# Optimization experiments

Hardware: AMD Instinct MI355X
Metric: run time of the kernel (lower is better)

## Reference

```python
import jax, jax.numpy as jnp
import numpy as np
import math

V, H, L, NH, I, E, K, S, B = 32000, 1024, 4, 16, 2816, 8, 2, 2048, 1
HD = H // NH
MOE_IDX = 2
EPS = 1e-6
THETA = 10000.0
AUX_COEF, Z_COEF = 0.01, 0.001


def setup_inputs() -> dict:
    key = jax.random.key(0)
    ks = jax.random.split(key, 20)
    std = 0.02
    n_dense = L - 1  # layers 0,1,3
    inp = {
        "input_ids": jax.random.randint(ks[0], (B, S), 0, V, dtype=jnp.int64),
        "embed": jax.random.normal(ks[1], (V, H), jnp.float32) * std,
        "ln1_w": jnp.ones((L, H), jnp.float32),
        "ln2_w": jnp.ones((L, H), jnp.float32),
        "wq": jax.random.normal(ks[2], (L, H, H), jnp.float32) * std,
        "wk": jax.random.normal(ks[3], (L, H, H), jnp.float32) * std,
        "wv": jax.random.normal(ks[4], (L, H, H), jnp.float32) * std,
        "wo": jax.random.normal(ks[5], (L, H, H), jnp.float32) * std,
        "dense_gate": jax.random.normal(ks[6], (n_dense, H, I), jnp.float32) * std,
        "dense_up": jax.random.normal(ks[7], (n_dense, H, I), jnp.float32) * std,
        "dense_down": jax.random.normal(ks[8], (n_dense, I, H), jnp.float32) * std,
        "router_w": jax.random.normal(ks[9], (H, E), jnp.float32) * std,
        "moe_gate": jax.random.normal(ks[10], (E, H, I), jnp.float32) * std,
        "moe_up": jax.random.normal(ks[11], (E, H, I), jnp.float32) * std,
        "moe_down": jax.random.normal(ks[12], (E, I, H), jnp.float32) * std,
        "final_norm_w": jnp.ones((H,), jnp.float32),
    }
    return inp


def rmsnorm(x, w):
    return x * jax.lax.rsqrt(jnp.mean(x * x, -1, keepdims=True) + EPS) * w


def rope_tables():
    inv_freq = 1.0 / (THETA ** (jnp.arange(0, HD, 2, dtype=jnp.float32) / HD))
    ang = jnp.arange(S, dtype=jnp.float32)[:, None] * inv_freq[None, :]  # [S, HD/2]
    return jnp.cos(ang), jnp.sin(ang)


def apply_rope(x, cos, sin):
    # x: [B,S,NH,HD]; cos/sin [S,HD/2] -> broadcast [1,S,1,HD/2]
    c = cos[None, :, None, :]
    s = sin[None, :, None, :]
    x1, x2 = jnp.split(x, 2, axis=-1)
    return jnp.concatenate([x1 * c - x2 * s, x2 * c + x1 * s], axis=-1)


def attention(x, wq, wk, wv, wo, cos, sin, mask):
    q = (x @ wq).reshape(B, S, NH, HD)
    k = (x @ wk).reshape(B, S, NH, HD)
    v = (x @ wv).reshape(B, S, NH, HD)
    q = apply_rope(q, cos, sin)
    k = apply_rope(k, cos, sin)
    scores = jnp.einsum("bqhd,bkhd->bhqk", q, k) / math.sqrt(HD)
    scores = jnp.where(mask, scores, jnp.finfo(scores.dtype).min)
    p = jax.nn.softmax(scores, axis=-1)
    o = jnp.einsum("bhqk,bkhd->bqhd", p, v).reshape(B, S, H)
    return o @ wo


def swiglu_mlp(x, wg, wu, wd):
    return (jax.nn.silu(x @ wg) * (x @ wu)) @ wd


def moe_layer(x, router_w, wg, wu, wd):
    T = B * S
    xf = x.reshape(T, H)
    rl = xf @ router_w  # [T,E]
    probs = jax.nn.softmax(rl, axis=-1)
    vals, idx = jax.lax.top_k(probs, K)  # [T,K]
    vals = vals / jnp.sum(vals, axis=-1, keepdims=True)
    rows = jnp.arange(T)[:, None]
    w = jnp.zeros((T, E), xf.dtype).at[rows, idx].set(vals)  # dense combine weights
    g = jnp.einsum("th,ehi->tei", xf, wg)
    u = jnp.einsum("th,ehi->tei", xf, wu)
    a = jax.nn.silu(g) * u
    y = jnp.einsum("tei,eih,te->th", a, wd, w)
    # load-balancing aux loss (Switch-style) + router z-loss
    sel = jnp.zeros((T, E), xf.dtype).at[rows, idx].add(1.0)
    f = jnp.mean(sel, axis=0)
    P = jnp.mean(probs, axis=0)
    aux = AUX_COEF * E * jnp.sum(f * P)
    z = Z_COEF * jnp.mean(jax.nn.logsumexp(rl, axis=-1) ** 2)
    return y.reshape(B, S, H), aux + z


def reference(input_ids, embed, ln1_w, ln2_w, wq, wk, wv, wo,
              dense_gate, dense_up, dense_down,
              router_w, moe_gate, moe_up, moe_down, final_norm_w):
    cos, sin = rope_tables()
    mask = jnp.tril(jnp.ones((S, S), bool))[None, None, :, :]
    h = embed[input_ids]  # [B,S,H]
    total_aux = jnp.float32(0.0)
    n_moe = 0
    d = 0  # dense layer counter
    for li in range(L):
        res = h
        hn = rmsnorm(h, ln1_w[li])
        h = res + attention(hn, wq[li], wk[li], wv[li], wo[li], cos, sin, mask)
        res = h
        hn = rmsnorm(h, ln2_w[li])
        if li == MOE_IDX:
            y, aux = moe_layer(hn, router_w, moe_gate, moe_up, moe_down)
            total_aux = total_aux + aux
            n_moe += 1
        else:
            y = swiglu_mlp(hn, dense_gate[d], dense_up[d], dense_down[d])
            d += 1
        h = res + y
    h = rmsnorm(h, final_norm_w)
    logits = h @ embed.T  # tied lm_head
    aux_loss = total_aux / n_moe
    return logits, aux_loss
```

## Files before the change

### kernel.cpp

```cpp
#include <hip/hip_runtime.h>
#include <hip/hip_bf16.h>
#include <math.h>

#define SEQ 2048
#define HID 1024
#define NHEAD 16
#define HDIM 64
#define IDIM 2816
#define NEXP 8
#define VOCAB 32000

#define ASTRIDE 144

typedef float f32x4v __attribute__((ext_vector_type(4)));
typedef __bf16 bf16x8v __attribute__((ext_vector_type(8)));
typedef __bf16 bf16x4v __attribute__((ext_vector_type(4)));

__device__ __forceinline__ bf16x8v cvt8(const float4& a, const float4& b) {
  bf16x8v r;
  r[0] = (__bf16)a.x; r[1] = (__bf16)a.y; r[2] = (__bf16)a.z; r[3] = (__bf16)a.w;
  r[4] = (__bf16)b.x; r[5] = (__bf16)b.y; r[6] = (__bf16)b.z; r[7] = (__bf16)b.w;
  return r;
}

#define MFMA(a, b, c) __builtin_amdgcn_mfma_f32_16x16x32_bf16(a, b, c, 0, 0, 0)

__device__ __forceinline__ void gld_lds16(const void* g, void* l) {
  __builtin_amdgcn_global_load_lds(
      (const __attribute__((address_space(1))) unsigned int*)(unsigned long long)g,
      (__attribute__((address_space(3))) unsigned int*)(unsigned int)(unsigned long long)l,
      16, 0, 0);
}

__global__ __launch_bounds__(256) void wsplit_t_kernel(
    const float* __restrict__ W, __bf16* __restrict__ WH, __bf16* __restrict__ WL,
    int K, int N)
{
  __shared__ float tile[64][65];
  const int tid = threadIdx.x;
  const size_t zofs = (size_t)blockIdx.z * K * N;
  const int n0 = blockIdx.x * 64, k0 = blockIdx.y * 64;
#pragma unroll
  for (int r = 0; r < 4; ++r) {
    int kk = (tid >> 4) + r * 16;
    int nn = (tid & 15) * 4;
    float4 v = *(const float4*)(W + zofs + (size_t)(k0 + kk) * N + n0 + nn);
    tile[kk][nn] = v.x; tile[kk][nn + 1] = v.y;
    tile[kk][nn + 2] = v.z; tile[kk][nn + 3] = v.w;
  }
  __syncthreads();
  const int nn = tid >> 2;
  const int kk = (tid & 3) * 16;
  __bf16* dh = WH + zofs + (size_t)(n0 + nn) * K + k0 + kk;
  __bf16* dl = WL + zofs + (size_t)(n0 + nn) * K + k0 + kk;
  bf16x8v h0, l0, h1, l1;
#pragma unroll
  for (int j = 0; j < 8; ++j) {
    float f = tile[kk + j][nn];
    __bf16 hb = (__bf16)f; h0[j] = hb; l0[j] = (__bf16)(f - (float)hb);
    f = tile[kk + 8 + j][nn];
    hb = (__bf16)f; h1[j] = hb; l1[j] = (__bf16)(f - (float)hb);
  }
  *(bf16x8v*)dh = h0; *(bf16x8v*)(dh + 8) = h1;
  *(bf16x8v*)dl = l0; *(bf16x8v*)(dl + 8) = l1;
}

__global__ __launch_bounds__(256) void wsplit_th_kernel(
    const float* __restrict__ W, __bf16* __restrict__ WH, int K, int N)
{
  __shared__ float tile[64][65];
  const int tid = threadIdx.x;
  const size_t zofs = (size_t)blockIdx.z * K * N;
  const int n0 = blockIdx.x * 64, k0 = blockIdx.y * 64;
#pragma unroll
  for (int r = 0; r < 4; ++r) {
    int kk = (tid >> 4) + r * 16;
    int nn = (tid & 15) * 4;
    float4 v = *(const float4*)(W + zofs + (size_t)(k0 + kk) * N + n0 + nn);
    tile[kk][nn] = v.x; tile[kk][nn + 1] = v.y;
    tile[kk][nn + 2] = v.z; tile[kk][nn + 3] = v.w;
  }
  __syncthreads();
  const int nn = tid >> 2;
  const int kk = (tid & 3) * 16;
  __bf16* dh = WH + zofs + (size_t)(n0 + nn) * K + k0 + kk;
  bf16x8v h0, h1;
#pragma unroll
  for (int j = 0; j < 8; ++j) {
    h0[j] = (__bf16)tile[kk + j][nn];
    h1[j] = (__bf16)tile[kk + 8 + j][nn];
  }
  *(bf16x8v*)dh = h0; *(bf16x8v*)(dh + 8) = h1;
}

__global__ __launch_bounds__(256) void esplit_kernel(
    const float* __restrict__ E, __bf16* __restrict__ EH)
{
  size_t i = ((size_t)blockIdx.x * 256 + threadIdx.x) * 8;
  float4 a = *(const float4*)(E + i);
  float4 b = *(const float4*)(E + i + 4);
  *(bf16x8v*)(EH + i) = cvt8(a, b);
}

template<bool COMP, bool ACCUM, int BM, int BN, bool XSWZ>
__global__ __launch_bounds__(256) void gemm_bt_kernel(
    const __bf16* __restrict__ Ah, const __bf16* __restrict__ Al,
    const __bf16* __restrict__ B0h, const __bf16* __restrict__ B0l,
    const __bf16* __restrict__ B1h, const __bf16* __restrict__ B1l,
    const __bf16* __restrict__ B2h, const __bf16* __restrict__ B2l,
    float* __restrict__ C0, float* __restrict__ C1, float* __restrict__ C2,
    int M, int N, int Kd)
{
  const __bf16* __restrict__ Bh = (blockIdx.z == 0) ? B0h : (blockIdx.z == 1 ? B1h : B2h);
  const __bf16* __restrict__ Bl = (blockIdx.z == 0) ? B0l : (blockIdx.z == 1 ? B1l : B2l);
  float* __restrict__ C         = (blockIdx.z == 0) ? C0 : (blockIdx.z == 1 ? C1 : C2);
  constexpr int ATILE = BM * 64;
  constexpr int BTILE = BN * 64;
  constexpr int MFR = BM / 32;
  constexpr int NFR = BN / 32;
  constexpr int SBUF = COMP ? 2 * (ATILE + BTILE) : (ATILE + BTILE);
  __shared__ __align__(16) char smem[2 * SBUF];
  const int tid = threadIdx.x;
  int bm, bn;
  if (XSWZ) {
    int id = blockIdx.x;
    int xcd = id & 7;
    int j = id >> 3;
    if (BM == 128) {
      bm = j & 15;
      bn = xcd * 32 + (j >> 4);
    } else {
      bm = j & 31;
      bn = xcd * 32 + (j >> 5);
    }
    if (bn >= N / BN) return;
  } else {
    bm = blockIdx.y;
// ... 13 lines not shown
#pragma unroll
    for (int c = wid; c < BM / 16; c += 4) {
      size_t gofs = (size_t)(bm * BM + c * 16 + lrow) * Kd + k0 + lcol;
      gld_lds16(Ah + gofs, AsH + c * 1024);
      if (COMP) gld_lds16(Al + gofs, AsL + c * 1024);
    }
#pragma unroll
    for (int c = wid; c < BN / 16; c += 4) {
      size_t gofs = (size_t)(bn * BN + c * 16 + lrow) * Kd + k0 + lcol;
      gld_lds16(Bh + gofs, BsH + c * 1024);
      if (COMP) gld_lds16(Bl + gofs, BsL + c * 1024);
    }
  };

  f32x4v acc[MFR][NFR];
  const f32x4v z4 = {0.f, 0.f, 0.f, 0.f};
#pragma unroll
  for (int i = 0; i < MFR; ++i)
#pragma unroll
    for (int j2 = 0; j2 < NFR; ++j2) acc[i][j2] = z4;

  stage(smem, 0);
  int cur = 0;
  for (int k0 = 0; k0 < Kd; k0 += 32) {
    __syncthreads();
    char* buf = smem + cur * SBUF;
    if (k0 + 32 < Kd) stage(smem + (cur ^ 1) * SBUF, k0 + 32);
    char* AsH = buf;
    char* BsH = buf + ATILE;
    char* AsL = COMP ? buf + ATILE + BTILE : buf;
    char* BsL = COMP ? buf + 2 * ATILE + BTILE : buf + ATILE;

    bf16x8v ah[MFR], al[MFR], bh4[NFR], bl4[NFR];
#pragma unroll
    for (int i = 0; i < MFR; ++i) {
      int r = wm + (i << 4) + lr;
      int off = r * 64 + (kh << 4);
      ah[i] = *(const bf16x8v*)(AsH + off);
      if (COMP) al[i] = *(const bf16x8v*)(AsL + off);
    }
#pragma unroll
    for (int i = 0; i < NFR; ++i) {
      int r = wn + (i << 4) + lr;
      int off = r * 64 + (kh << 4);
      bh4[i] = *(const bf16x8v*)(BsH + off);
      if (COMP) bl4[i] = *(const bf16x8v*)(BsL + off);
    }
#pragma unroll
    for (int mi = 0; mi < MFR; ++mi)
#pragma unroll
      for (int ni = 0; ni < NFR; ++ni) {
        if (COMP) {
          acc[mi][ni] = MFMA(al[mi], bh4[ni], acc[mi][ni]);
          acc[mi][ni] = MFMA(ah[mi], bl4[ni], acc[mi][ni]);
        }
        acc[mi][ni] = MFMA(ah[mi], bh4[ni], acc[mi][ni]);
      }
    cur ^= 1;
  }

  const int cr0 = kh << 2;
#pragma unroll
  for (int mi = 0; mi < MFR; ++mi)
#pragma unroll
    for (int ni = 0; ni < NFR; ++ni)
#pragma unroll
      for (int r = 0; r < 4; ++r) {
        int row = bm * BM + wm + (mi << 4) + cr0 + r;
        int col = bn * BN + wn + (ni << 4) + lr;
        size_t idx = (size_t)row * N + col;
        if (ACCUM) C[idx] += acc[mi][ni][r];
        else       C[idx] = acc[mi][ni][r];
      }
}

template<bool COMP>
__global__ __launch_bounds__(256) void gemm_qkv_kernel(
    const __bf16* __restrict__ Ah, const __bf16* __restrict__ Al,
    const __bf16* __restrict__ Bqh, const __bf16* __restrict__ Bql,
    const __bf16* __restrict__ Bkh, const __bf16* __restrict__ Bkl,
    const __bf16* __restrict__ Bvh, const __bf16* __restrict__ Bvl,
    __bf16* __restrict__ QH, __bf16* __restrict__ QL,
    __bf16* __restrict__ KH, __bf16* __restrict__ KL,
    float* __restrict__ Vout,
    const float* __restrict__ CT, const float* __restrict__ ST)
{
  const __bf16* __restrict__ Bh = (blockIdx.z == 0) ? Bqh : (blockIdx.z == 1 ? Bkh : Bvh);
  const __bf16* __restrict__ Bl = (blockIdx.z == 0) ? Bql : (blockIdx.z == 1 ? Bkl : Bvl);
  constexpr int ATILE = 64 * 64;
  constexpr int BTILE = 128 * 64;
  constexpr int SBUF = COMP ? 2 * (ATILE + BTILE) : (ATILE + BTILE);
  __shared__ __align__(16) char smem[2 * SBUF];
  const int tid = threadIdx.x;
  const int bm = blockIdx.y, bn = blockIdx.x;
  const int wid = tid >> 6, lane = tid & 63;
  const int wm = (wid >> 1) << 5, wn = (wid & 1) << 6;
  const int lr = lane & 15, kh = lane >> 4;
  const int lrow = lane >> 2;
  const int lcol = (lane & 3) << 3;

  auto stage = [&](char* buf, int k0) {
    char* AsH = buf;
    char* BsH = buf + ATILE;
    char* AsL = COMP ? buf + ATILE + BTILE : buf;
    char* BsL = COMP ? buf + 2 * ATILE + BTILE : buf + ATILE;
    {
      int c = wid;
      size_t gofs = (size_t)(bm * 64 + c * 16 + lrow) * HID + k0 + lcol;
      gld_lds16(Ah + gofs, AsH + c * 1024);
      if (COMP) gld_lds16(Al + gofs, AsL + c * 1024);
    }
#pragma unroll
    for (int c = wid; c < 8; c += 4) {
      size_t gofs = (size_t)(bn * 128 + c * 16 + lrow) * HID + k0 + lcol;
      gld_lds16(Bh + gofs, BsH + c * 1024);
      if (COMP) gld_lds16(Bl + gofs, BsL + c * 1024);
    }
  };

  f32x4v acc[2][4];
  const f32x4v z4 = {0.f, 0.f, 0.f, 0.f};
#pragma unroll
  for (int i = 0; i < 2; ++i)
#pragma unroll
    for (int j2 = 0; j2 < 4; ++j2) acc[i][j2] = z4;

  stage(smem, 0);
  int cur = 0;
  for (int k0 = 0; k0 < HID; k0 += 32) {
    __syncthreads();
    char* buf = smem + cur * SBUF;
    if (k0 + 32 < HID) stage(smem + (cur ^ 1) * SBUF, k0 + 32);
    char* AsH = buf;
    char* BsH = buf + ATILE;
    char* AsL = COMP ? buf + ATILE + BTILE : buf;
    char* BsL = COMP ? buf + 2 * ATILE + BTILE : buf + ATILE;

    bf16x8v ah2[2], al2[2], bh4[4], bl4[4];
#pragma unroll
    for (int i = 0; i < 2; ++i) {
      int r = wm + (i << 4) + lr;
      int off = r * 64 + (kh << 4);
      ah2[i] = *(const bf16x8v*)(AsH + off);
      if (COMP) al2[i] = *(const bf16x8v*)(AsL + off);
    }
#pragma unroll
    for (int i = 0; i < 4; ++i) {
      int r = wn + (i << 4) + lr;
      int off = r * 64 + (kh << 4);
      bh4[i] = *(const bf16x8v*)(BsH + off);
      if (COMP) bl4[i] = *(const bf16x8v*)(BsL + off);
    }
#pragma unroll
    for (int mi = 0; mi < 2; ++mi)
#pragma unroll
      for (int ni = 0; ni < 4; ++ni) {
        if (COMP) {
          acc[mi][ni] = MFMA(al2[mi], bh4[ni], acc[mi][ni]);
          acc[mi][ni] = MFMA(ah2[mi], bl4[ni], acc[mi][ni]);
        }
        acc[mi][ni] = MFMA(ah2[mi], bh4[ni], acc[mi][ni]);
      }
    cur ^= 1;
  }

  const int cr0 = kh << 2;
  if (blockIdx.z == 2) {
#pragma unroll
    for (int mi = 0; mi < 2; ++mi)
#pragma unroll
      for (int ni = 0; ni < 4; ++ni)
#pragma unroll
        for (int r = 0; r < 4; ++r) {
          int row = bm * 64 + wm + (mi << 4) + cr0 + r;
          int col = bn * 128 + wn + (ni << 4) + lr;
          Vout[(size_t)row * HID + col] = acc[mi][ni][r];
        }
  } else {
    const float scale = (blockIdx.z == 0) ? 0.125f : 1.0f;
    __bf16* OH = (blockIdx.z == 0) ? QH : KH;
    __bf16* OL = (blockIdx.z == 0) ? QL : KL;
#pragma unroll
    for (int mi = 0; mi < 2; ++mi)
#pragma unroll
      for (int ni = 0; ni < 2; ++ni)
#pragma unroll
        for (int r = 0; r < 4; ++r) {
          int row = bm * 64 + wm + (mi << 4) + cr0 + r;
          int col = bn * 128 + wn + (ni << 4) + lr;
          int i = col & 31;
          float c = CT[row * 32 + i], sn = ST[row * 32 + i];
          float x1 = acc[mi][ni][r];
          float x2 = acc[mi][ni + 2][r];
          float o1 = (x1 * c - x2 * sn) * scale;
          float o2 = (x2 * c + x1 * sn) * scale;
          size_t ofs = (size_t)row * HID + col;
          __bf16 h1 = (__bf16)o1;
          OH[ofs] = h1; OL[ofs] = (__bf16)(o1 - (float)h1);
          __bf16 h2 = (__bf16)o2;
          OH[ofs + 32] = h2; OL[ofs + 32] = (__bf16)(o2 - (float)h2);
        }
  }
}

template<bool COMP>
__global__ __launch_bounds__(256) void gemm_dgu_kernel(
    const __bf16* __restrict__ Ah, const __bf16* __restrict__ Al,
    const __bf16* __restrict__ BGh, const __bf16* __restrict__ BGl,
    const __bf16* __restrict__ BUh, const __bf16* __restrict__ BUl,
    __bf16* __restrict__ GH, __bf16* __restrict__ GL)
{
  constexpr int SBUF = COMP ? 24576 : 12288;
  __shared__ __align__(16) char smem[2 * SBUF];
  const int tid = threadIdx.x;
  const int bn = blockIdx.x, bm = blockIdx.y;
  const int wid = tid >> 6, lane = tid & 63;
  const int wm = (wid >> 1) << 5, wn = (wid & 1) << 5;
  const int lr = lane & 15, kh = lane >> 4;
  const int lrow = lane >> 2;
  const int lcol = (lane & 3) << 3;

  auto stage = [&](char* buf, int k0) {
    char* AsH = buf;
    char* BgH = buf + 4096;
    char* BuH = buf + 8192;
    char* AsL = COMP ? buf + 12288 : buf;
    char* BgL = COMP ? buf + 16384 : buf;
    char* BuL = COMP ? buf + 20480 : buf;
    int c = wid;
    size_t aofs = (size_t)(bm * 64 + c * 16 + lrow) * HID + k0 + lcol;
    gld_lds16(Ah + aofs, AsH + c * 1024);
    if (COMP) gld_lds16(Al + aofs, AsL + c * 1024);
    size_t bofs = (size_t)(bn * 64 + c * 16 + lrow) * HID + k0 + lcol;
    gld_lds16(BGh + bofs, BgH + c * 1024);
    gld_lds16(BUh + bofs, BuH + c * 1024);
    if (COMP) {
      gld_lds16(BGl + bofs, BgL + c * 1024);
      gld_lds16(BUl + bofs, BuL + c * 1024);
    }
  };

  f32x4v accg[2][2], accu[2][2];
  const f32x4v z4 = {0.f, 0.f, 0.f, 0.f};
#pragma unroll
  for (int i = 0; i < 2; ++i)
#pragma unroll
    for (int j = 0; j < 2; ++j) { accg[i][j] = z4; accu[i][j] = z4; }

  stage(smem, 0);
  int cur = 0;
  for (int k0 = 0; k0 < HID; k0 += 32) {
    __syncthreads();
    char* buf = smem + cur * SBUF;
    if (k0 + 32 < HID) stage(smem + (cur ^ 1) * SBUF, k0 + 32);
    char* AsH = buf;
    char* BgH = buf + 4096;
    char* BuH = buf + 8192;
    char* AsL = COMP ? buf + 12288 : buf;
    char* BgL = COMP ? buf + 16384 : buf;
    char* BuL = COMP ? buf + 20480 : buf;

    bf16x8v af[2], afl[2], bg4[2], bgl4[2], bu4[2], bul4[2];
#pragma unroll
    for (int i = 0; i < 2; ++i) {
      int r = wm + (i << 4) + lr;
      int off = r * 64 + (kh << 4);
      af[i] = *(const bf16x8v*)(AsH + off);
      if (COMP) afl[i] = *(const bf16x8v*)(AsL + off);
    }
#pragma unroll
    for (int i = 0; i < 2; ++i) {
      int r = wn + (i << 4) + lr;
      int off = r * 64 + (kh << 4);
      bg4[i] = *(const bf16x8v*)(BgH + off);
      bu4[i] = *(const bf16x8v*)(BuH + off);
      if (COMP) {
        bgl4[i] = *(const bf16x8v*)(BgL + off);
        bul4[i] = *(const bf16x8v*)(BuL + off);
      }
    }
#pragma unroll
    for (int mi = 0; mi < 2; ++mi)
#pragma unroll
      for (int ni = 0; ni < 2; ++ni) {
        if (COMP) {
          accg[mi][ni] = MFMA(afl[mi], bg4[ni], accg[mi][ni]);
          accg[mi][ni] = MFMA(af[mi], bgl4[ni], accg[mi][ni]);
        }
        accg[mi][ni] = MFMA(af[mi], bg4[ni], accg[mi][ni]);
        if (COMP) {
          accu[mi][ni] = MFMA(afl[mi], bu4[ni], accu[mi][ni]);
          accu[mi][ni] = MFMA(af[mi], bul4[ni], accu[mi][ni]);
        }
        accu[mi][ni] = MFMA(af[mi], bu4[ni], accu[mi][ni]);
      }
    cur ^= 1;
  }

  const int cr0 = kh << 2;
#pragma unroll
  for (int mi = 0; mi < 2; ++mi)
#pragma unroll
    for (int ni = 0; ni < 2; ++ni)
#pragma unroll
      for (int r = 0; r < 4; ++r) {
        int row = bm * 64 + wm + (mi << 4) + cr0 + r;
        int col = bn * 64 + wn + (ni << 4) + lr;
        float gv = accg[mi][ni][r];
        float uv = accu[mi][ni][r];
        float a = gv / (1.f + __expf(-gv)) * uv;
        size_t idx = (size_t)row * IDIM + col;
        __bf16 hb = (__bf16)a;
        GH[idx] = hb;
        GL[idx] = (__bf16)(a - (float)hb);
      }
}

__global__ __launch_bounds__(256) void vtsplit_kernel(
    const float* __restrict__ V, __bf16* __restrict__ VTH, __bf16* __restrict__ VTL)
{
  __shared__ float tile[64][65];
  const int tid = threadIdx.x;
  const int s0 = blockIdx.x * 64;
  const int head = blockIdx.y;
#pragma unroll
  for (int r = 0; r < 4; ++r) {
    int ss = (tid >> 4) + r * 16;
    int dd = (tid & 15) * 4;
    float4 v = *(const float4*)(V + (size_t)(s0 + ss) * HID + head * 64 + dd);
    tile[ss][dd] = v.x; tile[ss][dd + 1] = v.y;
    tile[ss][dd + 2] = v.z; tile[ss][dd + 3] = v.w;
  }
  __syncthreads();
#pragma unroll
  for (int half = 0; half < 2; ++half) {
    const int d = (tid >> 3) + (half << 5);
    const int c = tid & 7;
    bf16x8v hv, lv;
#pragma unroll
    for (int j = 0; j < 8; ++j) {
      float f = tile[c * 8 + j][d];
      __bf16 hb = (__bf16)f;
      hv[j] = hb; lv[j] = (__bf16)(f - (float)hb);
    }
    size_t dst = (size_t)(head * 64 + d) * SEQ + s0 + c * 8;
    *(bf16x8v*)(VTH + dst) = hv;
    *(bf16x8v*)(VTL + dst) = lv;
  }
}

__global__ __launch_bounds__(256) void attn_flash_kernel(
    const __bf16* __restrict__ QH, const __bf16* __restrict__ QL,
    const __bf16* __restrict__ KH, const __bf16* __restrict__ KL,
    const __bf16* __restrict__ VTH, const __bf16* __restrict__ VTL,
    __bf16* __restrict__ OH, __bf16* __restrict__ OL)
{
  const int head = blockIdx.y;
  const int tid = threadIdx.x, wid = tid >> 6, lane = tid & 63;
  const int lr = lane & 15, kh = lane >> 4;
  __shared__ __align__(16) char KsH[64 * ASTRIDE], KsL[64 * ASTRIDE];
  __shared__ __align__(16) char VtH[64 * ASTRIDE], VtL[64 * ASTRIDE];
  __shared__ __align__(16) char PsH[4][16 * ASTRIDE], PsL[4][16 * ASTRIDE];

#pragma unroll
  for (int seg = 0; seg < 2; ++seg) {
    const int qt = seg ? (31 - (int)blockIdx.x) : (int)blockIdx.x;

    const size_t qofs = (size_t)(qt * 64 + wid * 16 + lr) * HID + head * HDIM;
    const bf16x8v qfh0 = *(const bf16x8v*)(QH + qofs + (kh << 3));
    const bf16x8v qfh1 = *(const bf16x8v*)(QH + qofs + 32 + (kh << 3));
    const bf16x8v qfl0 = *(const bf16x8v*)(QL + qofs + (kh << 3));
    const bf16x8v qfl1 = *(const bf16x8v*)(QL + qofs + 32 + (kh << 3));

    float m_run[4], l_run[4];
    f32x4v oacc[4];
    const f32x4v z4 = {0.f, 0.f, 0.f, 0.f};
#pragma unroll
    for (int i = 0; i < 4; ++i) { m_run[i] = -1e30f; l_run[i] = 0.f; oacc[i] = z4; }

    for (int kt = 0; kt <= qt; ++kt) {
      __syncthreads();
#pragma unroll
      for (int p = 0; p < 2; ++p) {
        int g = tid + (p << 8);
        int r = g >> 3;
        int c = g & 7;
        int off = r * ASTRIDE + (c << 4);
        const size_t kofs = (size_t)(kt * 64 + r) * HID + head * HDIM + (c << 3);
        *(bf16x8v*)(KsH + off) = *(const bf16x8v*)(KH + kofs);
        *(bf16x8v*)(KsL + off) = *(const bf16x8v*)(KL + kofs);
        const size_t vofs = (size_t)(head * 64 + r) * SEQ + kt * 64 + (c << 3);
        *(bf16x8v*)(VtH + off) = *(const bf16x8v*)(VTH + vofs);
        *(bf16x8v*)(VtL + off) = *(const bf16x8v*)(VTL + vofs);
      }
      __syncthreads();

      float sv[4][4];
#pragma unroll
      for (int stt = 0; stt < 4; ++stt) {
        int r = (stt << 4) + lr;
        int off0 = r * ASTRIDE + (kh << 4);
        int off1 = off0 + 64;
        bf16x8v kfh0 = *(const bf16x8v*)(KsH + off0);
        bf16x8v kfl0 = *(const bf16x8v*)(KsL + off0);
        bf16x8v kfh1 = *(const bf16x8v*)(KsH + off1);
        bf16x8v kfl1 = *(const bf16x8v*)(KsL + off1);
        f32x4v s = z4;
        s = MFMA(qfl0, kfh0, s);
        s = MFMA(qfh0, kfl0, s);
        s = MFMA(qfh0, kfh0, s);
        s = MFMA(qfl1, kfh1, s);
        s = MFMA(qfh1, kfl1, s);
        s = MFMA(qfh1, kfh1, s);
        int key = kt * 64 + (stt << 4) + lr;
#pragma unroll
        for (int rr = 0; rr < 4; ++rr) {
          int qr = qt * 64 + wid * 16 + (kh << 2) + rr;
          sv[stt][rr] = (key <= qr) ? s[rr] : -1e30f;
        }
      }

#pragma unroll
      for (int rr = 0; rr < 4; ++rr) {
        float mx = fmaxf(fmaxf(sv[0][rr], sv[1][rr]), fmaxf(sv[2][rr], sv[3][rr]));
#pragma unroll
        for (int d = 1; d < 16; d <<= 1) mx = fmaxf(mx, __shfl_xor(mx, d));
        float mnew = fmaxf(m_run[rr], mx);
        float scl = __expf(m_run[rr] - mnew);
        float pv[4];
#pragma unroll
        for (int stt = 0; stt < 4; ++stt) pv[stt] = __expf(sv[stt][rr] - mnew);
        float rs = pv[0] + pv[1] + pv[2] + pv[3];
#pragma unroll
        for (int d = 1; d < 16; d <<= 1) rs += __shfl_xor(rs, d);
        l_run[rr] = l_run[rr] * scl + rs;
        m_run[rr] = mnew;
#pragma unroll
        for (int n = 0; n < 4; ++n) oacc[n][rr] *= scl;
        int qlr = (kh << 2) + rr;
#pragma unroll
        for (int stt = 0; stt < 4; ++stt) {
          __bf16 hb = (__bf16)pv[stt];
          __bf16 lb = (__bf16)(pv[stt] - (float)hb);
          int off = qlr * ASTRIDE + (((stt << 4) + lr) << 1);
          *(__bf16*)(PsH[wid] + off) = hb;
          *(__bf16*)(PsL[wid] + off) = lb;
        }
      }

      int poff0 = lr * ASTRIDE + (kh << 4);
      int poff1 = poff0 + 64;
      bf16x8v pah0 = *(const bf16x8v*)(PsH[wid] + poff0);
      bf16x8v pal0 = *(const bf16x8v*)(PsL[wid] + poff0);
      bf16x8v pah1 = *(const bf16x8v*)(PsH[wid] + poff1);
      bf16x8v pal1 = *(const bf16x8v*)(PsL[wid] + poff1);
#pragma unroll
      for (int n = 0; n < 4; ++n) {
        int vr = (n << 4) + lr;
        int voff0 = vr * ASTRIDE + (kh << 4);
        int voff1 = voff0 + 64;
        bf16x8v vfh0 = *(const bf16x8v*)(VtH + voff0);
        bf16x8v vfl0 = *(const bf16x8v*)(VtL + voff0);
        bf16x8v vfh1 = *(const bf16x8v*)(VtH + voff1);
        bf16x8v vfl1 = *(const bf16x8v*)(VtL + voff1);
        oacc[n] = MFMA(pal0, vfh0, oacc[n]);
        oacc[n] = MFMA(pah0, vfl0, oacc[n]);
        oacc[n] = MFMA(pah0, vfh0, oacc[n]);
        oacc[n] = MFMA(pal1, vfh1, oacc[n]);
        oacc[n] = MFMA(pah1, vfl1, oacc[n]);
        oacc[n] = MFMA(pah1, vfh1, oacc[n]);
      }
    }

#pragma unroll
    for (int n = 0; n < 4; ++n)
#pragma unroll
      for (int rr = 0; rr < 4; ++rr) {
        int qr = qt * 64 + wid * 16 + (kh << 2) + rr;
        size_t ofs = (size_t)qr * HID + head * HDIM + (n << 4) + lr;
        float val = oacc[n][rr] / l_run[rr];
        __bf16 hb = (__bf16)val;
        OH[ofs] = hb;
        OL[ofs] = (__bf16)(val - (float)hb);
      }
  }
}

__global__ __launch_bounds__(256) void gemm_moe_guf_kernel(
    const __bf16* __restrict__ Xh,
    const __bf16* __restrict__ MGH, const __bf16* __restrict__ MUH,
    __bf16* __restrict__ A2, const float* __restrict__ W,
    const int* __restrict__ list, const int* __restrict__ cnt8,
    const int* __restrict__ off8)
{
  const int e = blockIdx.z;
  const int cnt = cnt8[e];
  const int bn = blockIdx.x, bm = blockIdx.y;
  if (bm * 128 >= cnt) return;
  const int base = off8[e];
  constexpr int SBUF = 16384;
  __shared__ __align__(16) char smem[2 * SBUF];
  const int tid = threadIdx.x;
  const int wid = tid >> 6, lane = tid & 63;
  const int wm = (wid >> 1) << 6, wn = (wid & 1) << 5;
  const int lr = lane & 15, kh = lane >> 4;
  const int lrow = lane >> 2;
  const int lcol = (lane & 3) << 3;

  auto stage = [&](char* buf, int k0) {
    char* AsB = buf;
    char* BgB = buf + 8192;
    char* BuB = buf + 12288;
#pragma unroll
    for (int c = wid; c < 8; c += 4) {
      int rg = bm * 128 + c * 16 + lrow;
      int tok = list[e * SEQ + (rg < cnt ? rg : cnt - 1)];
      gld_lds16(Xh + (size_t)tok * HID + k0 + lcol, AsB + c * 1024);
    }
    {
      int c = wid;
      size_t wofs = (size_t)(e * IDIM + bn * 64 + c * 16 + lrow) * HID + k0 + lcol;
      gld_lds16(MGH + wofs, BgB + c * 1024);
      gld_lds16(MUH + wofs, BuB + c * 1024);
    }
  };

  f32x4v accg[4][2], accu[4][2];
  const f32x4v z4 = {0.f, 0.f, 0.f, 0.f};
#pragma unroll
  for (int i = 0; i < 4; ++i)
#pragma unroll
    for (int j = 0; j < 2; ++j) { accg[i][j] = z4; accu[i][j] = z4; }

  stage(smem, 0);
  int cur = 0;
  for (int k0 = 0; k0 < HID; k0 += 32) {
    __syncthreads();
    char* buf = smem + cur * SBUF;
    if (k0 + 32 < HID) stage(smem + (cur ^ 1) * SBUF, k0 + 32);
    char* AsB = buf;
    char* BgB = buf + 8192;
    char* BuB = buf + 12288;

    bf16x8v af[4], bg4[2], bu4[2];
#pragma unroll
    for (int i = 0; i < 4; ++i) {
      int r = wm + (i << 4) + lr;
      af[i] = *(const bf16x8v*)(AsB + r * 64 + (kh << 4));
    }
#pragma unroll
    for (int i = 0; i < 2; ++i) {
      int r = wn + (i << 4) + lr;
      bg4[i] = *(const bf16x8v*)(BgB + r * 64 + (kh << 4));
      bu4[i] = *(const bf16x8v*)(BuB + r * 64 + (kh << 4));
// ... 71 lines not shown
    for (int j = 0; j < 2; ++j) acc[i][j] = z4;

  stage(smem, 0);
  int cur = 0;
  for (int k0 = 0; k0 < IDIM; k0 += 32) {
    __syncthreads();
    char* buf = smem + cur * SBUF;
    if (k0 + 32 < IDIM) stage(smem + (cur ^ 1) * SBUF, k0 + 32);
    char* AsB = buf;
    char* BsB = buf + 8192;

    bf16x8v af[4], bfv[2];
#pragma unroll
    for (int i = 0; i < 4; ++i) {
      int r = wm + (i << 4) + lr;
      af[i] = *(const bf16x8v*)(AsB + r * 64 + (kh << 4));
    }
#pragma unroll
    for (int i = 0; i < 2; ++i) {
      int r = wn + (i << 4) + lr;
      bfv[i] = *(const bf16x8v*)(BsB + r * 64 + (kh << 4));
    }
#pragma unroll
    for (int mi = 0; mi < 4; ++mi)
#pragma unroll
      for (int ni = 0; ni < 2; ++ni)
        acc[mi][ni] = MFMA(af[mi], bfv[ni], acc[mi][ni]);
    cur ^= 1;
  }

  const int cr0 = kh << 2;
#pragma unroll
  for (int mi = 0; mi < 4; ++mi)
#pragma unroll
    for (int ni = 0; ni < 2; ++ni)
#pragma unroll
      for (int r = 0; r < 4; ++r) {
        int row = bm * 128 + wm + (mi << 4) + cr0 + r;
        if (row < cnt) {
          int col = bn * 64 + wn + (ni << 4) + lr;
          Y2[(size_t)(base + row) * HID + col] = acc[mi][ni][r];
        }
      }
}

__global__ __launch_bounds__(256) void moe_scatter_kernel(
    const int* __restrict__ tokpair, const int* __restrict__ off8,
    const float* __restrict__ Y2, float* __restrict__ H)
{
  const int t = blockIdx.x;
  const int i = threadIdx.x;
  int p0 = tokpair[t * 2], p1 = tokpair[t * 2 + 1];
  size_t r0 = off8[p0 >> 16] + (p0 & 0xffff);
  size_t r1 = off8[p1 >> 16] + (p1 & 0xffff);
  float4 a = ((const float4*)(Y2 + r0 * HID))[i];
  float4 b = ((const float4*)(Y2 + r1 * HID))[i];
  float4 hv = ((float4*)(H + (size_t)t * HID))[i];
  hv.x = (hv.x + a.x) + b.x;
  hv.y = (hv.y + a.y) + b.y;
  hv.z = (hv.z + a.z) + b.z;
  hv.w = (hv.w + a.w) + b.w;
  ((float4*)(H + (size_t)t * HID))[i] = hv;
}

__global__ void tables_kernel(float* __restrict__ CT, float* __restrict__ ST)
{
  int idx = blockIdx.x * 256 + threadIdx.x;
  int s = idx >> 5, i = idx & 31;
  double inv = exp(-log(10000.0) * (double)i / 32.0);
  double ang = (double)s * inv;
  CT[idx] = (float)cos(ang);
  ST[idx] = (float)sin(ang);
}

__global__ __launch_bounds__(256) void embed_kernel(
    const int* __restrict__ ids, const float* __restrict__ E, float* __restrict__ H)
{
  int t = blockIdx.x;
  int id = ids[t];
  ((float4*)(H + (size_t)t * HID))[threadIdx.x] =
      ((const float4*)(E + (size_t)id * HID))[threadIdx.x];
}

__global__ __launch_bounds__(256) void rmsnorm_kernel(
    const float* __restrict__ X, const float* __restrict__ W,
    float* __restrict__ O, __bf16* __restrict__ OHb, __bf16* __restrict__ OLb)
{
  int t = blockIdx.x;
  int tid = threadIdx.x;
  float4 v = ((const float4*)(X + (size_t)t * HID))[tid];
  float ss = v.x * v.x + v.y * v.y + v.z * v.z + v.w * v.w;
#pragma unroll
  for (int d = 1; d < 64; d <<= 1) ss += __shfl_xor(ss, d);
  __shared__ float red[4];
  if ((tid & 63) == 0) red[tid >> 6] = ss;
  __syncthreads();
  float tot = red[0] + red[1] + red[2] + red[3];
  float inv = 1.0f / sqrtf(tot * (1.0f / 1024.0f) + 1e-6f);
  float4 w = ((const float4*)W)[tid];
  float4 r;
  r.x = v.x * inv * w.x; r.y = v.y * inv * w.y;
  r.z = v.z * inv * w.z; r.w = v.w * inv * w.w;
  ((float4*)(O + (size_t)t * HID))[tid] = r;
  float f[4] = {r.x, r.y, r.z, r.w};
  bf16x4v hv, lv;
#pragma unroll
  for (int j = 0; j < 4; ++j) {
    __bf16 hb = (__bf16)f[j];
    hv[j] = hb; lv[j] = (__bf16)(f[j] - (float)hb);
  }
  *(bf16x4v*)(OHb + (size_t)t * HID + tid * 4) = hv;
  *(bf16x4v*)(OLb + (size_t)t * HID + tid * 4) = lv;
}

__global__ __launch_bounds__(256) void router_kernel(
    const float* __restrict__ X, const float* __restrict__ RW, float* __restrict__ RL)
{
  int wid = threadIdx.x >> 6, lane = threadIdx.x & 63;
  int t = blockIdx.x * 4 + wid;
  const float* x = X + (size_t)t * HID;
  float a0 = 0, a1 = 0, a2 = 0, a3 = 0, a4 = 0, a5 = 0, a6 = 0, a7 = 0;
  for (int hh = lane; hh < HID; hh += 64) {
    float xv = x[hh];
    float4 f0 = *(const float4*)(RW + hh * 8);
    float4 f1 = *(const float4*)(RW + hh * 8 + 4);
    a0 += xv * f0.x; a1 += xv * f0.y; a2 += xv * f0.z; a3 += xv * f0.w;
    a4 += xv * f1.x; a5 += xv * f1.y; a6 += xv * f1.z; a7 += xv * f1.w;
  }
#pragma unroll
  for (int d = 1; d < 64; d <<= 1) {
    a0 += __shfl_xor(a0, d); a1 += __shfl_xor(a1, d);
    a2 += __shfl_xor(a2, d); a3 += __shfl_xor(a3, d);
    a4 += __shfl_xor(a4, d); a5 += __shfl_xor(a5, d);
    a6 += __shfl_xor(a6, d); a7 += __shfl_xor(a7, d);
  }
  if (lane == 0) {
    float* dst = RL + (size_t)t * 8;
    dst[0] = a0; dst[1] = a1; dst[2] = a2; dst[3] = a3;
    dst[4] = a4; dst[5] = a5; dst[6] = a6; dst[7] = a7;
  }
}

__global__ void zero_kernel(float* __restrict__ p, int n)
{
  int i = threadIdx.x;
  if (i < n) p[i] = 0.f;
}

__global__ void zeroi_kernel(int* __restrict__ p, int n)
{
  int i = threadIdx.x;
  if (i < n) p[i] = 0;
}

__global__ __launch_bounds__(256) void topk_kernel(
    const float* __restrict__ RL, float* __restrict__ W, float* __restrict__ AUX)
{
  int t = blockIdx.x * 256 + threadIdx.x;
  int lane = threadIdx.x & 63;
  float r[8];
#pragma unroll
  for (int e = 0; e < 8; ++e) r[e] = RL[t * 8 + e];
  float mx = r[0];
#pragma unroll
  for (int e = 1; e < 8; ++e) mx = fmaxf(mx, r[e]);
  float p[8];
  float se = 0.f;
#pragma unroll
  for (int e = 0; e < 8; ++e) { p[e] = __expf(r[e] - mx); se += p[e]; }
  float inv = 1.f / se;
#pragma unroll
  for (int e = 0; e < 8; ++e) p[e] *= inv;
  float lse = logf(se) + mx;
  int i1 = 0; float v1 = p[0];
#pragma unroll
  for (int e = 1; e < 8; ++e) if (p[e] > v1) { v1 = p[e]; i1 = e; }
  int i2 = -1; float v2 = -1.f;
#pragma unroll
  for (int e = 0; e < 8; ++e) if (e != i1 && p[e] > v2) { v2 = p[e]; i2 = e; }
  float s12 = v1 + v2;
#pragma unroll
  for (int e = 0; e < 8; ++e)
    W[t * 8 + e] = (e == i1) ? v1 / s12 : ((e == i2) ? v2 / s12 : 0.f);
#pragma unroll
  for (int e = 0; e < 8; ++e) {
    float fe = ((i1 == e) ? 1.f : 0.f) + ((i2 == e) ? 1.f : 0.f);
// ... 36 lines not shown
  }
}

__global__ void prefix_kernel(const int* __restrict__ cnt, int* __restrict__ off)
{
  if (threadIdx.x == 0) {
    int s = 0;
    for (int e = 0; e < 8; ++e) { off[e] = s; s += cnt[e]; }
  }
}

extern "C" void kernel_launch(void* const* d_in, const int* in_sizes, int n_in,
                              void* d_out, int out_size, void* d_ws, size_t ws_size,
                              hipStream_t stream)
{
  const int*   ids   = (const int*)d_in[0];
  const float* embed = (const float*)d_in[1];
  const float* ln1   = (const float*)d_in[2];
  const float* ln2   = (const float*)d_in[3];
  const float* wq    = (const float*)d_in[4];
  const float* wk    = (const float*)d_in[5];
  const float* wv    = (const float*)d_in[6];
  const float* wo    = (const float*)d_in[7];
  const float* dg    = (const float*)d_in[8];
  const float* du    = (const float*)d_in[9];
  const float* dd    = (const float*)d_in[10];
  const float* rw    = (const float*)d_in[11];
  const float* mg    = (const float*)d_in[12];
  const float* mu    = (const float*)d_in[13];
  const float* md    = (const float*)d_in[14];
  const float* fin   = (const float*)d_in[15];
  float* out = (float*)d_out;

  char* ws = (char*)d_ws;
  float* h    = (float*)(ws + 0);
  float* hn   = (float*)(ws + 8388608);
  float* q    = (float*)(ws + 16777216);
  float* k    = (float*)(ws + 25165824);
  float* v    = (float*)(ws + 33554432);
  __bf16* oh  = (__bf16*)(ws + 41943040);
  __bf16* ol  = (__bf16*)(ws + 46137344);
  float* g    = (float*)(ws + 50331648);
  float* u    = (float*)(ws + 73400320);
  float* ct   = (float*)(ws + 96468992);
  float* st   = (float*)(ws + 96731136);
  float* rl   = (float*)(ws + 96993280);
  float* wmoe = (float*)(ws + 97058816);
  float* aux  = (float*)(ws + 97124352);
  int*   cnt  = (int*)  (ws + 97124608);
  int*   list = (int*)  (ws + 97124864);
  int*   tokp = (int*)  (ws + 97190400);
  int*   off8 = (int*)  (ws + 97206784);
  __bf16* wqh = (__bf16*)(ws + 97320960);
  __bf16* wql = (__bf16*)(ws + 105709568);
  __bf16* wkh = (__bf16*)(ws + 114098176);
  __bf16* wkl = (__bf16*)(ws + 122486784);
  __bf16* wvh = (__bf16*)(ws + 130875392);
  __bf16* wvl = (__bf16*)(ws + 139264000);
  __bf16* woh = (__bf16*)(ws + 147652608);
  __bf16* wol = (__bf16*)(ws + 156041216);
  __bf16* dgh = (__bf16*)(ws + 164429824);
  __bf16* dgl = (__bf16*)(ws + 181731328);
  __bf16* duh = (__bf16*)(ws + 199032832);
  __bf16* dul = (__bf16*)(ws + 216334336);
  __bf16* ddh = (__bf16*)(ws + 233635840);
  __bf16* ddl = (__bf16*)(ws + 250937344);
  __bf16* eh  = (__bf16*)(ws + 268238848);
  __bf16* hnh = (__bf16*)(ws + 333774848);
  __bf16* hnl = (__bf16*)(ws + 337969152);
  __bf16* gh  = (__bf16*)(ws + 342163456);
  __bf16* gl  = (__bf16*)(ws + 353697792);
  __bf16* mgh = (__bf16*)(ws + 365232128);
  __bf16* muh = (__bf16*)(ws + 411369472);
  __bf16* mdh = (__bf16*)(ws + 457506816);
  __bf16* qh  = (__bf16*)g;
  __bf16* ql  = (__bf16*)((char*)g + 4194304);
  __bf16* kbh = (__bf16*)((char*)g + 8388608);
  __bf16* kbl = (__bf16*)((char*)g + 12582912);
  __bf16* vth = (__bf16*)u;
  __bf16* vtl = (__bf16*)((char*)u + 4194304);
  __bf16* a2  = (__bf16*)g;
  float*  y2  = u;

  wsplit_t_kernel<<<dim3(16, 16, 4), 256, 0, stream>>>(wq, wqh, wql, HID, HID);
  wsplit_t_kernel<<<dim3(16, 16, 4), 256, 0, stream>>>(wk, wkh, wkl, HID, HID);
  wsplit_t_kernel<<<dim3(16, 16, 4), 256, 0, stream>>>(wv, wvh, wvl, HID, HID);
  wsplit_t_kernel<<<dim3(16, 16, 4), 256, 0, stream>>>(wo, woh, wol, HID, HID);
  wsplit_t_kernel<<<dim3(44, 16, 3), 256, 0, stream>>>(dg, dgh, dgl, HID, IDIM);
  wsplit_t_kernel<<<dim3(44, 16, 3), 256, 0, stream>>>(du, duh, dul, HID, IDIM);
  wsplit_t_kernel<<<dim3(16, 44, 3), 256, 0, stream>>>(dd, ddh, ddl, IDIM, HID);
  wsplit_th_kernel<<<dim3(44, 16, 8), 256, 0, stream>>>(mg, mgh, HID, IDIM);
  wsplit_th_kernel<<<dim3(44, 16, 8), 256, 0, stream>>>(mu, muh, HID, IDIM);
  wsplit_th_kernel<<<dim3(16, 44, 8), 256, 0, stream>>>(md, mdh, IDIM, HID);
  esplit_kernel<<<16000, 256, 0, stream>>>(embed, eh);

  tables_kernel<<<256, 256, 0, stream>>>(ct, st);
  embed_kernel<<<SEQ, 256, 0, stream>>>(ids, embed, h);

  for (int li = 0; li < 4; ++li) {
    const bool comp = (li <= 2);
    rmsnorm_kernel<<<SEQ, 256, 0, stream>>>(h, ln1 + li * HID, hn, hnh, hnl);
    size_t wofs = (size_t)li * HID * HID;
    if (comp)
      gemm_qkv_kernel<true><<<dim3(8, 32, 3), 256, 0, stream>>>(
          hnh, hnl, wqh + wofs, wql + wofs, wkh + wofs, wkl + wofs,
          wvh + wofs, wvl + wofs, qh, ql, kbh, kbl, v, ct, st);
    else
      gemm_qkv_kernel<false><<<dim3(8, 32, 3), 256, 0, stream>>>(
          hnh, hnh, wqh + wofs, wqh + wofs, wkh + wofs, wkh + wofs,
          wvh + wofs, wvh + wofs, qh, ql, kbh, kbl, v, ct, st);

    vtsplit_kernel<<<dim3(32, 16), 256, 0, stream>>>(v, vth, vtl);

    attn_flash_kernel<<<dim3(16, 16), 256, 0, stream>>>(
        qh, ql, kbh, kbl, vth, vtl, oh, ol);

    if (comp)
      gemm_bt_kernel<true, true, 64, 64, false><<<dim3(16, 32, 1), 256, 0, stream>>>(
          oh, ol, woh + wofs, wol + wofs, woh + wofs, wol + wofs,
          woh + wofs, wol + wofs, h, h, h, SEQ, HID, HID);
    else
      gemm_bt_kernel<false, true, 64, 64, false><<<dim3(16, 32, 1), 256, 0, stream>>>(
          oh, oh, woh + wofs, woh + wofs, woh + wofs, woh + wofs,
          woh + wofs, woh + wofs, h, h, h, SEQ, HID, HID);

    rmsnorm_kernel<<<SEQ, 256, 0, stream>>>(h, ln2 + li * HID, hn, hnh, hnl);
    if (li == 2) {
      router_kernel<<<512, 256, 0, stream>>>(hn, rw, rl);
      zero_kernel<<<1, 32, 0, stream>>>(aux, 17);
      topk_kernel<<<8, 256, 0, stream>>>(rl, wmoe, aux);
      aux_kernel<<<1, 1, 0, stream>>>(aux, out);
      zeroi_kernel<<<1, 32, 0, stream>>>(cnt, 8);
      build_list_kernel<<<8, 256, 0, stream>>>(wmoe, cnt, list, tokp);
      prefix_kernel<<<1, 64, 0, stream>>>(cnt, off8);
      gemm_moe_guf_kernel<<<dim3(44, 16, 8), 256, 0, stream>>>(
          hnh, mgh, muh, a2, wmoe, list, cnt, off8);
      gemm_moe_down2_kernel<<<dim3(16, 16, 8), 256, 0, stream>>>(
          a2, mdh, y2, cnt, off8);
      moe_scatter_kernel<<<SEQ, 256, 0, stream>>>(tokp, off8, y2, h);
    } else {
      int d = (li < 2) ? li : li - 1;
      size_t go = (size_t)d * HID * IDIM;
      if (comp)
        gemm_dgu_kernel<true><<<dim3(44, 32), 256, 0, stream>>>(
            hnh, hnl, dgh + go, dgl + go, duh + go, dul + go, gh, gl);
      else
        gemm_dgu_kernel<false><<<dim3(44, 32), 256, 0, stream>>>(
            hnh, hnh, dgh + go, dgh + go, duh + go, duh + go, gh, gl);
      if (comp)
        gemm_bt_kernel<true, true, 64, 64, false><<<dim3(16, 32, 1), 256, 0, stream>>>(
            gh, gl, ddh + go, ddl + go, ddh + go, ddl + go,
            ddh + go, ddl + go, h, h, h, SEQ, HID, IDIM);
      else
        gemm_bt_kernel<false, true, 64, 64, false><<<dim3(16, 32, 1), 256, 0, stream>>>(
            gh, gh, ddh + go, ddh + go, ddh + go, ddh + go,
            ddh + go, ddh + go, h, h, h, SEQ, HID, IDIM);
    }
  }
  rmsnorm_kernel<<<SEQ, 256, 0, stream>>>(h, fin, hn, hnh, hnl);
  gemm_bt_kernel<false, false, 128, 128, true><<<dim3(4096, 1, 1), 256, 0, stream>>>(
      hnh, hnh, eh, eh, eh, eh, eh, eh, out, out, out, SEQ, VOCAB, HID);
}
```

Measured before the change: 1.711 ms.

## Fuse V transpose-split into QKV GEMM, merge weight splits, trim rmsnorm writes

The V projection epilogue now goes through LDS, transposes, and writes the bf16 hi/lo V^T buffers itself, so the separate vtsplit kernel and the fp32 V round trip are gone. The four per-matrix Q/K/V/O weight split launches become one kernel launch. rmsnorm skips its fp32 output except where the router needs it. s_setprio hints are added around the MFMA sections in the attention kernel. The shared-memory buffer grows to 32KB for the non-compensated variant, which can lower occupancy, and the hardcoded byte offsets in the weight split assume a contiguous buffer layout.

```diff
diff --git a/kernel.cpp b/kernel.cpp
--- a/kernel.cpp
+++ b/kernel.cpp
@@ -53,6 +53,45 @@
   const int kk = (tid & 3) * 16;
   __bf16* dh = WH + zofs + (size_t)(n0 + nn) * K + k0 + kk;
   __bf16* dl = WL + zofs + (size_t)(n0 + nn) * K + k0 + kk;
+  bf16x8v h0, l0, h1, l1;
+#pragma unroll
+  for (int j = 0; j < 8; ++j) {
+    float f = tile[kk + j][nn];
+    __bf16 hb = (__bf16)f; h0[j] = hb; l0[j] = (__bf16)(f - (float)hb);
+    f = tile[kk + 8 + j][nn];
+    hb = (__bf16)f; h1[j] = hb; l1[j] = (__bf16)(f - (float)hb);
+  }
+  *(bf16x8v*)dh = h0; *(bf16x8v*)(dh + 8) = h1;
+  *(bf16x8v*)dl = l0; *(bf16x8v*)(dl + 8) = l1;
+}
+
+__global__ __launch_bounds__(256) void wsplit_qkvo_kernel(
+    const float* __restrict__ W0, const float* __restrict__ W1,
+    const float* __restrict__ W2, const float* __restrict__ W3,
+    __bf16* __restrict__ WHbase)
+{
+  const int z = blockIdx.z;
+  const int li = z & 3, sel = z >> 2;
+  const float* W = (sel == 0) ? W0 : (sel == 1) ? W1 : (sel == 2) ? W2 : W3;
+  const size_t lofs = (size_t)li * HID * HID;
+  __bf16* WH = (__bf16*)((char*)WHbase + (size_t)sel * 16777216) + lofs;
+  __bf16* WL = (__bf16*)((char*)WHbase + (size_t)sel * 16777216 + 8388608) + lofs;
+  __shared__ float tile[64][65];
+  const int tid = threadIdx.x;
+  const int n0 = blockIdx.x * 64, k0 = blockIdx.y * 64;
+#pragma unroll
+  for (int r = 0; r < 4; ++r) {
+    int kk = (tid >> 4) + r * 16;
+    int nn = (tid & 15) * 4;
+    float4 v = *(const float4*)(W + lofs + (size_t)(k0 + kk) * HID + n0 + nn);
+    tile[kk][nn] = v.x; tile[kk][nn + 1] = v.y;
+    tile[kk][nn + 2] = v.z; tile[kk][nn + 3] = v.w;
+  }
+  __syncthreads();
+  const int nn = tid >> 2;
+  const int kk = (tid & 3) * 16;
+  __bf16* dh = WH + (size_t)(n0 + nn) * HID + k0 + kk;
+  __bf16* dl = WL + (size_t)(n0 + nn) * HID + k0 + kk;
   bf16x8v h0, l0, h1, l1;
 #pragma unroll
   for (int j = 0; j < 8; ++j) {
@@ -232,7 +271,7 @@
     const __bf16* __restrict__ Bvh, const __bf16* __restrict__ Bvl,
     __bf16* __restrict__ QH, __bf16* __restrict__ QL,
     __bf16* __restrict__ KH, __bf16* __restrict__ KL,
-    float* __restrict__ Vout,
+    __bf16* __restrict__ VTH, __bf16* __restrict__ VTL,
     const float* __restrict__ CT, const float* __restrict__ ST)
 {
   const __bf16* __restrict__ Bh = (blockIdx.z == 0) ? Bqh : (blockIdx.z == 1 ? Bkh : Bvh);
@@ -240,7 +279,8 @@
   constexpr int ATILE = 64 * 64;
   constexpr int BTILE = 128 * 64;
   constexpr int SBUF = COMP ? 2 * (ATILE + BTILE) : (ATILE + BTILE);
-  __shared__ __align__(16) char smem[2 * SBUF];
+  constexpr int SMEMSZ = (2 * SBUF > 32768) ? 2 * SBUF : 32768;
+  __shared__ __align__(16) char smem[SMEMSZ];
   const int tid = threadIdx.x;
   const int bm = blockIdx.y, bn = blockIdx.x;
   const int wid = tid >> 6, lane = tid & 63;
@@ -316,16 +356,35 @@
 
   const int cr0 = kh << 2;
   if (blockIdx.z == 2) {
+    float* tf = (float*)smem;
+    __syncthreads();
 #pragma unroll
     for (int mi = 0; mi < 2; ++mi)
 #pragma unroll
       for (int ni = 0; ni < 4; ++ni)
 #pragma unroll
         for (int r = 0; r < 4; ++r) {
-          int row = bm * 64 + wm + (mi << 4) + cr0 + r;
-          int col = bn * 128 + wn + (ni << 4) + lr;
-          Vout[(size_t)row * HID + col] = acc[mi][ni][r];
+          int rrow = wm + (mi << 4) + cr0 + r;
+          int ccol = wn + (ni << 4) + lr;
+          tf[rrow * 128 + ccol] = acc[mi][ni][r];
         }
+    __syncthreads();
+#pragma unroll
+    for (int t4 = 0; t4 < 4; ++t4) {
+      int idx = tid + (t4 << 8);
+      int d = idx >> 3;
+      int c = idx & 7;
+      bf16x8v hv, lv;
+#pragma unroll
+      for (int j = 0; j < 8; ++j) {
+        float f = tf[(c * 8 + j) * 128 + d];
+        __bf16 hb = (__bf16)f;
+        hv[j] = hb; lv[j] = (__bf16)(f - (float)hb);
+      }
+      size_t dst = (size_t)(bn * 128 + d) * SEQ + bm * 64 + c * 8;
+      *(bf16x8v*)(VTH + dst) = hv;
+      *(bf16x8v*)(VTL + dst) = lv;
+    }
   } else {
     const float scale = (blockIdx.z == 0) ? 0.125f : 1.0f;
     __bf16* OH = (blockIdx.z == 0) ? QH : KH;
@@ -466,39 +525,6 @@
       }
 }
 
-__global__ __launch_bounds__(256) void vtsplit_kernel(
-    const float* __restrict__ V, __bf16* __restrict__ VTH, __bf16* __restrict__ VTL)
-{
-  __shared__ float tile[64][65];
-  const int tid = threadIdx.x;
-  const int s0 = blockIdx.x * 64;
-  const int head = blockIdx.y;
-#pragma unroll
-  for (int r = 0; r < 4; ++r) {
-    int ss = (tid >> 4) + r * 16;
-    int dd = (tid & 15) * 4;
-    float4 v = *(const float4*)(V + (size_t)(s0 + ss) * HID + head * 64 + dd);
-    tile[ss][dd] = v.x; tile[ss][dd + 1] = v.y;
-    tile[ss][dd + 2] = v.z; tile[ss][dd + 3] = v.w;
-  }
-  __syncthreads();
-#pragma unroll
-  for (int half = 0; half < 2; ++half) {
-    const int d = (tid >> 3) + (half << 5);
-    const int c = tid & 7;
-    bf16x8v hv, lv;
-#pragma unroll
-    for (int j = 0; j < 8; ++j) {
-      float f = tile[c * 8 + j][d];
-      __bf16 hb = (__bf16)f;
-      hv[j] = hb; lv[j] = (__bf16)(f - (float)hb);
-    }
-    size_t dst = (size_t)(head * 64 + d) * SEQ + s0 + c * 8;
-    *(bf16x8v*)(VTH + dst) = hv;
-    *(bf16x8v*)(VTL + dst) = lv;
-  }
-}
-
 __global__ __launch_bounds__(256) void attn_flash_kernel(
     const __bf16* __restrict__ QH, const __bf16* __restrict__ QL,
     const __bf16* __restrict__ KH, const __bf16* __restrict__ KL,
@@ -546,6 +572,7 @@
       __syncthreads();
 
       float sv[4][4];
+      __builtin_amdgcn_s_setprio(1);
 #pragma unroll
       for (int stt = 0; stt < 4; ++stt) {
         int r = (stt << 4) + lr;
@@ -569,6 +596,7 @@
           sv[stt][rr] = (key <= qr) ? s[rr] : -1e30f;
         }
       }
+      __builtin_amdgcn_s_setprio(0);
 
 #pragma unroll
       for (int rr = 0; rr < 4; ++rr) {
@@ -604,6 +632,7 @@
       bf16x8v pal0 = *(const bf16x8v*)(PsL[wid] + poff0);
       bf16x8v pah1 = *(const bf16x8v*)(PsH[wid] + poff1);
       bf16x8v pal1 = *(const bf16x8v*)(PsL[wid] + poff1);
+      __builtin_amdgcn_s_setprio(1);
 #pragma unroll
       for (int n = 0; n < 4; ++n) {
         int vr = (n << 4) + lr;
@@ -620,6 +649,7 @@
         oacc[n] = MFMA(pah1, vfl1, oacc[n]);
         oacc[n] = MFMA(pah1, vfh1, oacc[n]);
       }
+      __builtin_amdgcn_s_setprio(0);
     }
 
 #pragma unroll
@@ -857,6 +887,7 @@
       ((const float4*)(E + (size_t)id * HID))[threadIdx.x];
 }
 
+template<bool WF32>
 __global__ __launch_bounds__(256) void rmsnorm_kernel(
     const float* __restrict__ X, const float* __restrict__ W,
     float* __restrict__ O, __bf16* __restrict__ OHb, __bf16* __restrict__ OLb)
@@ -876,7 +907,7 @@
   float4 r;
   r.x = v.x * inv * w.x; r.y = v.y * inv * w.y;
   r.z = v.z * inv * w.z; r.w = v.w * inv * w.w;
-  ((float4*)(O + (size_t)t * HID))[tid] = r;
+  if (WF32) ((float4*)(O + (size_t)t * HID))[tid] = r;
   float f[4] = {r.x, r.y, r.z, r.w};
   bf16x4v hv, lv;
 #pragma unroll
@@ -1079,10 +1110,7 @@
   __bf16* a2  = (__bf16*)g;
   float*  y2  = u;
 
-  wsplit_t_kernel<<<dim3(16, 16, 4), 256, 0, stream>>>(wq, wqh, wql, HID, HID);
-  wsplit_t_kernel<<<dim3(16, 16, 4), 256, 0, stream>>>(wk, wkh, wkl, HID, HID);
-  wsplit_t_kernel<<<dim3(16, 16, 4), 256, 0, stream>>>(wv, wvh, wvl, HID, HID);
-  wsplit_t_kernel<<<dim3(16, 16, 4), 256, 0, stream>>>(wo, woh, wol, HID, HID);
+  wsplit_qkvo_kernel<<<dim3(16, 16, 16), 256, 0, stream>>>(wq, wk, wv, wo, wqh);
   wsplit_t_kernel<<<dim3(44, 16, 3), 256, 0, stream>>>(dg, dgh, dgl, HID, IDIM);
   wsplit_t_kernel<<<dim3(44, 16, 3), 256, 0, stream>>>(du, duh, dul, HID, IDIM);
   wsplit_t_kernel<<<dim3(16, 44, 3), 256, 0, stream>>>(dd, ddh, ddl, IDIM, HID);
@@ -1096,18 +1124,16 @@
 
   for (int li = 0; li < 4; ++li) {
     const bool comp = (li <= 2);
-    rmsnorm_kernel<<<SEQ, 256, 0, stream>>>(h, ln1 + li * HID, hn, hnh, hnl);
+    rmsnorm_kernel<false><<<SEQ, 256, 0, stream>>>(h, ln1 + li * HID, hn, hnh, hnl);
     size_t wofs = (size_t)li * HID * HID;
     if (comp)
       gemm_qkv_kernel<true><<<dim3(8, 32, 3), 256, 0, stream>>>(
           hnh, hnl, wqh + wofs, wql + wofs, wkh + wofs, wkl + wofs,
-          wvh + wofs, wvl + wofs, qh, ql, kbh, kbl, v, ct, st);
+          wvh + wofs, wvl + wofs, qh, ql, kbh, kbl, vth, vtl, ct, st);
     else
       gemm_qkv_kernel<false><<<dim3(8, 32, 3), 256, 0, stream>>>(
           hnh, hnh, wqh + wofs, wqh + wofs, wkh + wofs, wkh + wofs,
-          wvh + wofs, wvh + wofs, qh, ql, kbh, kbl, v, ct, st);
-
-    vtsplit_kernel<<<dim3(32, 16), 256, 0, stream>>>(v, vth, vtl);
+          wvh + wofs, wvh + wofs, qh, ql, kbh, kbl, vth, vtl, ct, st);
 
     attn_flash_kernel<<<dim3(16, 16), 256, 0, stream>>>(
         qh, ql, kbh, kbl, vth, vtl, oh, ol);
@@ -1121,8 +1147,8 @@
           oh, oh, woh + wofs, woh + wofs, woh + wofs, woh + wofs,
           woh + wofs, woh + wofs, h, h, h, SEQ, HID, HID);
 
-    rmsnorm_kernel<<<SEQ, 256, 0, stream>>>(h, ln2 + li * HID, hn, hnh, hnl);
     if (li == 2) {
+      rmsnorm_kernel<true><<<SEQ, 256, 0, stream>>>(h, ln2 + li * HID, hn, hnh, hnl);
       router_kernel<<<512, 256, 0, stream>>>(hn, rw, rl);
       zero_kernel<<<1, 32, 0, stream>>>(aux, 17);
       topk_kernel<<<8, 256, 0, stream>>>(rl, wmoe, aux);
@@ -1136,6 +1162,7 @@
           a2, mdh, y2, cnt, off8);
       moe_scatter_kernel<<<SEQ, 256, 0, stream>>>(tokp, off8, y2, h);
     } else {
+      rmsnorm_kernel<false><<<SEQ, 256, 0, stream>>>(h, ln2 + li * HID, hn, hnh, hnl);
       int d = (li < 2) ? li : li - 1;
       size_t go = (size_t)d * HID * IDIM;
       if (comp)
@@ -1154,7 +1181,7 @@
             ddh + go, ddh + go, h, h, h, SEQ, HID, IDIM);
     }
   }
-  rmsnorm_kernel<<<SEQ, 256, 0, stream>>>(h, fin, hn, hnh, hnl);
+  rmsnorm_kernel<false><<<SEQ, 256, 0, stream>>>(h, fin, hn, hnh, hnl);
   gemm_bt_kernel<false, false, 128, 128, true><<<dim3(4096, 1, 1), 256, 0, stream>>>(
       hnh, hnh, eh, eh, eh, eh, eh, eh, out, out, out, SEQ, VOCAB, HID);
 }
```

After: 1.668 ms. 2.5% less time.
